# Kernel tuning notes

Measured on AMD Instinct MI355X. Metric: run time of the kernel, lower is better.

Reference implementation:

```python
import jax, jax.numpy as jnp
import numpy as np

B, T, D, H, L, W = 32, 512, 256, 8, 2, 10
NQ = 10000
HD = D // H


def setup_inputs():
    key = jax.random.key(0)
    ks = jax.random.split(key, 16)
    def n(k, shape, s=0.02):
        return jax.random.normal(k, shape, jnp.float32) * s
    return {
        "q": jax.random.randint(ks[0], (B, T), 0, NQ),
        "s": jax.random.randint(ks[1], (B, T), 0, 2),
        "q_embed": n(ks[2], (NQ + 1, D)),
        "s_embed": n(ks[3], (2, D)),
        "pos_embed": n(ks[4], (512, D)),
        "fusion_w": n(ks[5], (2 * D, D)),
        "fusion_b": jnp.zeros((D,), jnp.float32),
        "in_proj_w": n(ks[6], (L, D, 3 * D)),
        "in_proj_b": jnp.zeros((L, 3 * D), jnp.float32),
        "out_proj_w": n(ks[7], (L, D, D)),
        "out_proj_b": jnp.zeros((L, D), jnp.float32),
        "ln1_g": jnp.ones((L, D), jnp.float32),
        "ln1_b": jnp.zeros((L, D), jnp.float32),
        "ln2_g": jnp.ones((L, D), jnp.float32),
        "ln2_b": jnp.zeros((L, D), jnp.float32),
        "ff1_w": n(ks[8], (L, D, 4 * D)),
        "ff1_b": jnp.zeros((L, 4 * D), jnp.float32),
        "ff2_w": n(ks[9], (L, 4 * D, D)),
        "ff2_b": jnp.zeros((L, D), jnp.float32),
        "sw1": n(ks[10], (6, 32), 0.1),
        "sb1": jnp.zeros((32,), jnp.float32),
        "sw2": n(ks[11], (32, D // 4), 0.1),
        "sb2": jnp.zeros((D // 4,), jnp.float32),
        "cw1": n(ks[12], (D + D // 4, D)),
        "cb1": jnp.zeros((D,), jnp.float32),
        "cw2": n(ks[13], (D, 1)),
        "cb2": jnp.zeros((1,), jnp.float32),
    }


def _ln(x, g, b):
    mu = jnp.mean(x, -1, keepdims=True)
    var = jnp.mean(jnp.square(x - mu), -1, keepdims=True)
    return (x - mu) * jax.lax.rsqrt(var + 1e-5) * g + b


def _sliding_sum(x, w):
    # sum over trailing window of size w ending at each t, via prefix sums
    c = jnp.concatenate([jnp.zeros((x.shape[0], 1), x.dtype), jnp.cumsum(x, axis=1)], axis=1)
    t = jnp.arange(x.shape[1])
    return c[:, t + 1] - c[:, jnp.maximum(t + 1 - w, 0)]


def _stats(s, mask):
    # vectorized version of _extract_statistics (prefix-sum sliding windows)
    mf = mask.astype(jnp.float32)
    sf = s.astype(jnp.float32) * mf
    valid = _sliding_sum(mf, W)
    correct_rate = _sliding_sum(sf, W) / (valid + 1e-6)
    rc = _sliding_sum(mf, 5)
    recent_correct = _sliding_sum(sf, 5) / (rc + 1e-6)
    trans = ((s[:, 1:] != s[:, :-1]) & mask[:, 1:] & mask[:, :-1]).astype(jnp.float32)
    diff = jnp.concatenate([jnp.zeros((s.shape[0], 1), jnp.float32), trans], axis=1)
    change_rate = _sliding_sum(diff, W - 1) / (valid + 1e-6)
    # max consecutive equal run within each trailing window of size W
    sp = jnp.pad(s, ((0, 0), (W - 1, 0)))
    mp = jnp.pad(mask, ((0, 0), (W - 1, 0)))
    win_s = [sp[:, j:j + T] for j in range(W)]
    win_m = [mp[:, j:j + T] for j in range(W)]
    run = win_m[0].astype(jnp.float32)
    mx = run
    for j in range(1, W):  # fixed small window, not a data-dim loop
        eq = (win_s[j] == win_s[j - 1]) & win_m[j - 1]
        run = win_m[j].astype(jnp.float32) * (jnp.where(eq, run, 0.0) + 1.0)
        mx = jnp.maximum(mx, run)
    rel = jnp.broadcast_to(jnp.arange(T, dtype=jnp.float32) / max(T, 100), s.shape)
    cov = valid / W
    return jnp.stack([correct_rate, recent_correct, change_rate, mx / W, rel, cov], axis=-1)


def reference(q, s, q_embed, s_embed, pos_embed, fusion_w, fusion_b, in_proj_w, in_proj_b,
              out_proj_w, out_proj_b, ln1_g, ln1_b, ln2_g, ln2_b, ff1_w, ff1_b, ff2_w, ff2_b,
              sw1, sb1, sw2, sb2, cw1, cb1, cw2, cb2):
    mask = s >= 0
    qm = jnp.where(mask, q, 0)
    sm = jnp.where(mask, s, 0)
    h = jnp.concatenate([q_embed[qm], s_embed[sm]], axis=-1)  # [B,T,2D]
    h = jax.nn.relu(h @ fusion_w + fusion_b) + pos_embed[:T][None]
    causal = jnp.tril(jnp.ones((T, T), bool))
    allowed = causal[None, None] & mask[:, None, None, :]
    scale = 1.0 / (HD ** 0.5)
    for l in range(L):
        qkv = h @ in_proj_w[l] + in_proj_b[l]
        qh, kh, vh = jnp.split(qkv, 3, axis=-1)
        qh = qh.reshape(B, T, H, HD).transpose(0, 2, 1, 3)
        kh = kh.reshape(B, T, H, HD).transpose(0, 2, 1, 3)
        vh = vh.reshape(B, T, H, HD).transpose(0, 2, 1, 3)
        scores = jnp.einsum('bhqd,bhkd->bhqk', qh, kh) * scale
        scores = jnp.where(allowed, scores, -1e9)
        attn = jax.nn.softmax(scores, axis=-1)
        o = jnp.einsum('bhqk,bhkd->bhqd', attn, vh).transpose(0, 2, 1, 3).reshape(B, T, D)
        h = _ln(h + (o @ out_proj_w[l] + out_proj_b[l]), ln1_g[l], ln1_b[l])
        ff = jax.nn.gelu(h @ ff1_w[l] + ff1_b[l], approximate=False) @ ff2_w[l] + ff2_b[l]
        h = _ln(h + ff, ln2_g[l], ln2_b[l])
    sfeat = _stats(sm, mask)  # [B,T,6]
    semb = jax.nn.relu(sfeat @ sw1 + sb1) @ sw2 + sb2  # [B,T,D//4]
    comb = jnp.concatenate([h, semb], axis=-1)
    logits = (jax.nn.relu(comb @ cw1 + cb1) @ cw2 + cb2)[..., 0]
    return jnp.where(mask, logits, -1e9)
```

## Files before the change

kernel.cpp:

```cpp
#include <hip/hip_runtime.h>
#include <hip/hip_bf16.h>
#include <cmath>


using short8 = __attribute__((ext_vector_type(8))) short;
using short4v = __attribute__((ext_vector_type(4))) short;
using f32x4  = __attribute__((ext_vector_type(4))) float;

__device__ inline float gelu_f(float x) {
    return 0.5f * x * (1.0f + erff(x * 0.70710678118654752f));
}

__device__ inline short f2bf(float x) {
    union { float f; unsigned u; } v; v.f = x;
    return (short)((v.u + 0x7fffu + ((v.u >> 16) & 1u)) >> 16);
}

__device__ inline float bf2f(short v) {
    union { unsigned u; float f; } x; x.u = ((unsigned)(unsigned short)v) << 16;
    return x.f;
}

__device__ inline unsigned packbf(float lo, float hi) {
    union { float f; unsigned u; } a, b; a.f = lo; b.f = hi;
    unsigned ra = (a.u + 0x7fffu + ((a.u >> 16) & 1u)) >> 16;
    unsigned rb = (b.u + 0x7fffu + ((b.u >> 16) & 1u)) >> 16;
    return (rb << 16) | (ra & 0xffffu);
}

#define GLOAD16(gp, lp) __builtin_amdgcn_global_load_lds( \
    (const __attribute__((address_space(1))) void*)(gp), \
    (__attribute__((address_space(3))) void*)(lp), 16, 0, 0)

__global__ __launch_bounds__(256) void prep_kernel(
    const float* __restrict__ fusion_w, const float* __restrict__ in_proj_w,
    const float* __restrict__ out_proj_w, const float* __restrict__ ff1_w,
    const float* __restrict__ ff2_w, const float* __restrict__ cw1,
    short* __restrict__ wts,
    const int* __restrict__ q, const int* __restrict__ s,
    const float* __restrict__ qe, const float* __restrict__ se,
    short* __restrict__ A)
{
    __shared__ float tile[32][33];
    if (blockIdx.x < 1744) {
        const int b0[10]      = {0,128,320,512,576,640,896,1152,1408,1664};
        const int Ks[10]      = {512,256,256,256,256,256,256,1024,1024,320};
        const int Ns[10]      = {256,768,768,256,256,1024,1024,256,256,256};
        const int sidx[10]    = {0,1,1,2,2,3,3,4,4,5};
        const size_t soff[10] = {0,0,196608,0,65536,0,262144,0,262144,0};
        const size_t doff[10] = {0,131072,327680,524288,589824,655360,917504,1179648,1441792,1703936};
        const float* srcs[6] = {fusion_w, in_proj_w, out_proj_w, ff1_w, ff2_w, cw1};
        int bid = blockIdx.x;
        int mi = 0;
        while (mi < 9 && bid >= b0[mi + 1]) ++mi;
        int bl = bid - b0[mi];
        int K = Ks[mi], N = Ns[mi];
        int tx = bl % (N >> 5), ty = bl / (N >> 5);
        const float* src = srcs[sidx[mi]] + soff[mi];
        short* dst = wts + doff[mi];
        int c = threadIdx.x & 31, r = threadIdx.x >> 5;
#pragma unroll
        for (int i = 0; i < 4; ++i)
            tile[r + i * 8][c] = src[(size_t)(ty * 32 + r + i * 8) * N + tx * 32 + c];
        __syncthreads();
#pragma unroll
        for (int i = 0; i < 4; ++i)
            dst[(size_t)(tx * 32 + r + i * 8) * K + ty * 32 + c] = f2bf(tile[c][r + i * 8]);
    } else {
        int e8 = (blockIdx.x - 1744) * 256 + threadIdx.x;
        int row = e8 >> 6;
        int k8 = (e8 & 63) << 3;
        int sv = s[row];
        bool mk = sv >= 0;
        const float* src = (k8 < 256) ? qe + (size_t)(mk ? q[row] : 0) * 256 + k8
                                      : se + (size_t)(mk ? sv : 0) * 256 + (k8 - 256);
        float4 v0 = *(const float4*)src;
        float4 v1 = *(const float4*)(src + 4);
        short8 o;
        o[0] = f2bf(v0.x); o[1] = f2bf(v0.y); o[2] = f2bf(v0.z); o[3] = f2bf(v0.w);
        o[4] = f2bf(v1.x); o[5] = f2bf(v1.y); o[6] = f2bf(v1.z); o[7] = f2bf(v1.w);
        *(short8*)(A + (size_t)row * 512 + k8) = o;
    }
}

template<int EPI, int BN, int K>
__global__ __launch_bounds__(512) void gemm_bstat(
    const short* __restrict__ A, const short* __restrict__ Wt,
    const float* __restrict__ bias, short* __restrict__ out0,
    short* __restrict__ ok, short* __restrict__ ov,
    const float* __restrict__ pos)
{
    constexpr int SPR = K / 8;
    constexpr int NSTEP = K / 32;
    constexpr int NJ = BN / 16;
    __shared__ short Bs[BN * K];
    const int tid = threadIdx.x, lane = tid & 63, wv = tid >> 6;
    const int lg = lane >> 4, lr = lane & 15;
    const int n0 = blockIdx.y * BN;
    const int row0 = blockIdx.x * 128 + wv * 16;

#pragma unroll
    for (int i = 0; i < (BN * K) / 4096; ++i) {
        int slot = i * 512 + tid;
        int n = slot / SPR, posn = slot % SPR;
        int g = posn ^ (n & 7);
        GLOAD16(Wt + (size_t)(n0 + n) * K + g * 8, &Bs[slot * 8]);
    }
    const short* arow = A + (size_t)(row0 + lr) * K;
    short8 af[NSTEP];
#pragma unroll
    for (int kk = 0; kk < NSTEP; ++kk)
        af[kk] = *(const short8*)(arow + kk * 32 + lg * 8);
    __syncthreads();

    f32x4 acc[NJ] = {};
#pragma unroll
    for (int kk = 0; kk < NSTEP; ++kk) {
#pragma unroll
        for (int j = 0; j < NJ; ++j) {
            int n = j * 16 + lr;
            short8 b = *(const short8*)&Bs[n * K + (((kk * 4 + lg) ^ (n & 7)) << 3)];
            acc[j] = __builtin_amdgcn_mfma_f32_16x16x32_bf16(af[kk], b, acc[j], 0, 0, 0);
        }
    }

    if constexpr (EPI == 0) {
#pragma unroll
        for (int j = 0; j < NJ; ++j)
#pragma unroll
        for (int r = 0; r < 4; ++r) {
            int row = row0 + lg * 4 + r;
            int col = n0 + j * 16 + lr;
            float x = acc[j][r] + bias[col];
            x = fmaxf(x, 0.f) + pos[(size_t)(row & 511) * 256 + col];
            out0[(size_t)row * 256 + col] = f2bf(x);
        }
    } else if constexpr (EPI == 1) {
#pragma unroll
        for (int j = 0; j < NJ; ++j)
#pragma unroll
        for (int r = 0; r < 4; ++r) {
            int row = row0 + lg * 4 + r;
            int gcol = n0 + j * 16 + lr;
            int t = row & 511, bg = row >> 9;
            int sec = gcol >> 8, cc = gcol & 255;
            int h = cc >> 5, d = cc & 31, bh = bg * 8 + h;
            short v = f2bf(acc[j][r] + bias[gcol]);
            if (sec == 0)      out0[((size_t)bh * 512 + t) * 32 + d] = v;
            else if (sec == 1) ok[((size_t)bh * 512 + t) * 32 + d] = v;
            else {
                int kl = t & 31;
                ov[(size_t)bh * 16384 + (size_t)(t >> 5) * 1024 +
                   (size_t)((kl >> 2) & 3) * 256 + d * 8 + (((kl & 3) << 1) | ((kl >> 4) & 1))] = v;
            }
        }
    } else {
#pragma unroll
        for (int j = 0; j < NJ; ++j)
#pragma unroll
        for (int r = 0; r < 4; ++r) {
            int row = row0 + lg * 4 + r;
            int gcol = n0 + j * 16 + lr;
            float x = acc[j][r] + bias[gcol];
            out0[(size_t)row * 1024 + gcol] = f2bf(gelu_f(x));
        }
    }
}

template<int EPI>
__global__ __launch_bounds__(512) void gemm_red(
    const short* __restrict__ A, const short* __restrict__ A2,
    const short* __restrict__ Wt, const float* __restrict__ bias,
    short* __restrict__ hb,
    const float* __restrict__ gamma, const float* __restrict__ beta,
    const float* __restrict__ cw2, const float* __restrict__ cb2,
    const int* __restrict__ smask, float* __restrict__ outlog, int K)
{
    const int tid = threadIdx.x, lane = tid & 63, wv = tid >> 6;
    const int lg = lane >> 4, lr = lane & 15;
    const int wr = wv >> 2, wc = wv & 3;
    const int m0 = blockIdx.x * 64;

    __shared__ short As[2][2048];
    __shared__ short Bs[2][8192];
    __shared__ float redS[64][4];
    __shared__ float redQ[64][4];

    f32x4 acc[2][4] = {};
    const int nsteps = K >> 5;

    auto stage = [&](int buf, int step) {
        int k0 = step << 5;
        if (tid < 256) {
            int k = k0 + wv * 8;
            const short* srcA;
            if constexpr (EPI == 4)
                srcA = (k < 256) ? A + (size_t)(m0 + lane) * 256 + k
                                 : A2 + (size_t)(m0 + lane) * 64 + (k - 256);
            else
                srcA = A + (size_t)(m0 + lane) * K + k;
            GLOAD16(srcA, &As[buf][(wv * 64) * 8]);
        }
        {
            GLOAD16(Wt + (size_t)(tid & 255) * K + k0 + (tid >> 8) * 8,
                    &Bs[buf][(wv * 64) * 8]);
        }
        {
            int slot = tid + 512;
            GLOAD16(Wt + (size_t)(slot & 255) * K + k0 + (slot >> 8) * 8,
                    &Bs[buf][((wv + 8) * 64) * 8]);
        }
    };

    stage(0, 0);
    __syncthreads();
    for (int step = 0; step < nsteps; ++step) {
        int cur = step & 1;
        if (step + 1 < nsteps) stage(cur ^ 1, step + 1);
        short8 a[2], b[4];
#pragma unroll
        for (int i = 0; i < 2; ++i)
            a[i] = *(const short8*)&As[cur][(lg * 64 + wr * 32 + i * 16 + lr) * 8];
#pragma unroll
        for (int j = 0; j < 4; ++j)
            b[j] = *(const short8*)&Bs[cur][(lg * 256 + wc * 64 + j * 16 + lr) * 8];
#pragma unroll
        for (int i = 0; i < 2; ++i)
#pragma unroll
            for (int j = 0; j < 4; ++j)
                acc[i][j] = __builtin_amdgcn_mfma_f32_16x16x32_bf16(a[i], b[j], acc[i][j], 0, 0, 0);
        __syncthreads();
    }

    if constexpr (EPI == 3) {
        float ps[2][4], pq[2][4];
#pragma unroll
        for (int i = 0; i < 2; ++i)
#pragma unroll
        for (int r = 0; r < 4; ++r) { ps[i][r] = 0.f; pq[i][r] = 0.f; }
#pragma unroll
        for (int i = 0; i < 2; ++i)
#pragma unroll
        for (int j = 0; j < 4; ++j)
#pragma unroll
        for (int r = 0; r < 4; ++r) {
            int row = m0 + wr * 32 + i * 16 + lg * 4 + r;
            int col = wc * 64 + j * 16 + lr;
            float x = acc[i][j][r] + bias[col] + bf2f(hb[(size_t)row * 256 + col]);
            acc[i][j][r] = x;
            ps[i][r] += x; pq[i][r] += x * x;
        }
#pragma unroll
        for (int off = 1; off < 16; off <<= 1)
#pragma unroll
            for (int i = 0; i < 2; ++i)
#pragma unroll
            for (int r = 0; r < 4; ++r) {
                ps[i][r] += __shfl_xor(ps[i][r], off);
                pq[i][r] += __shfl_xor(pq[i][r], off);
            }
        if (lr == 0) {
#pragma unroll
            for (int i = 0; i < 2; ++i)
#pragma unroll
            for (int r = 0; r < 4; ++r) {
                int rl = wr * 32 + i * 16 + lg * 4 + r;
                redS[rl][wc] = ps[i][r]; redQ[rl][wc] = pq[i][r];
            }
        }
        __syncthreads();
#pragma unroll
        for (int i = 0; i < 2; ++i)
#pragma unroll
        for (int r = 0; r < 4; ++r) {
            int rl = wr * 32 + i * 16 + lg * 4 + r;
            int row = m0 + rl;
            float sm = redS[rl][0] + redS[rl][1] + redS[rl][2] + redS[rl][3];
            float sq = redQ[rl][0] + redQ[rl][1] + redQ[rl][2] + redQ[rl][3];
            float mu = sm * (1.f / 256.f);
            float var = sq * (1.f / 256.f) - mu * mu;
            float rstd = rsqrtf(var + 1e-5f);
#pragma unroll
            for (int j = 0; j < 4; ++j) {
                int col = wc * 64 + j * 16 + lr;
                float yv = (acc[i][j][r] - mu) * rstd * gamma[col] + beta[col];
                hb[(size_t)row * 256 + col] = f2bf(yv);
            }
        }
    } else {
        float pa[2][4];
#pragma unroll
        for (int i = 0; i < 2; ++i)
#pragma unroll
        for (int r = 0; r < 4; ++r) pa[i][r] = 0.f;
#pragma unroll
        for (int i = 0; i < 2; ++i)
#pragma unroll
        for (int j = 0; j < 4; ++j)
#pragma unroll
        for (int r = 0; r < 4; ++r) {
            int col = wc * 64 + j * 16 + lr;
            float x = fmaxf(acc[i][j][r] + bias[col], 0.f);
            pa[i][r] += x * cw2[col];
        }
#pragma unroll
        for (int off = 1; off < 16; off <<= 1)
#pragma unroll
            for (int i = 0; i < 2; ++i)
#pragma unroll
            for (int r = 0; r < 4; ++r) pa[i][r] += __shfl_xor(pa[i][r], off);
        if (lr == 0) {
#pragma unroll
            for (int i = 0; i < 2; ++i)
#pragma unroll
            for (int r = 0; r < 4; ++r)
                redS[wr * 32 + i * 16 + lg * 4 + r][wc] = pa[i][r];
        }
        __syncthreads();
        if (tid < 64) {
            int row = m0 + tid;
            float v = redS[tid][0] + redS[tid][1] + redS[tid][2] + redS[tid][3] + cb2[0];
            outlog[row] = (smask[row] >= 0) ? v : -1e9f;
        }
    }
}

__global__ __launch_bounds__(256) void attn_mfma(
    const short* __restrict__ Qg, const short* __restrict__ Kg,
    const short* __restrict__ VTg, short* __restrict__ O)
{
    __shared__ unsigned Wp[4][16][20];
    const int bh = blockIdx.x >> 2, part = blockIdx.x & 3;
    const int b = bh >> 3, h = bh & 7;
    const int wv = threadIdx.x >> 6, lane = threadIdx.x & 63;
    const int lg = lane >> 4, lr = lane & 15;
    const int slot = part * 4 + wv;
    const short* Qbh = Qg + (size_t)bh * 16384;
    const short* Kbh = Kg + (size_t)bh * 16384;
    const short* Vbh = VTg + (size_t)bh * 16384;
    const float scale = 0.17677669529663687f;

    for (int half = 0; half < 2; ++half) {
        const int tile = half ? (31 - slot) : slot;
        const int q0 = tile << 4;
        short8 qa = *(const short8*)(Qbh + (size_t)(q0 + lr) * 32 + lg * 8);
        f32x4 o0 = {}, o1 = {};
        float l_[4] = {0.f, 0.f, 0.f, 0.f};
        const int nfull = q0 >> 5;

        for (int c = 0; c <= nfull; ++c) {
            int kc = c << 5;
            short8 kf0 = *(const short8*)(Kbh + (size_t)(kc + lr) * 32 + lg * 8);
            short8 kf1 = *(const short8*)(Kbh + (size_t)(kc + 16 + lr) * 32 + lg * 8);
            f32x4 s0 = {}, s1 = {};
            s0 = __builtin_amdgcn_mfma_f32_16x16x32_bf16(qa, kf0, s0, 0, 0, 0);
            s1 = __builtin_amdgcn_mfma_f32_16x16x32_bf16(qa, kf1, s1, 0, 0, 0);
            float p0[4], p1[4];
            if (c < nfull) {
#pragma unroll
                for (int r = 0; r < 4; ++r) {
                    p0[r] = __expf(s0[r] * scale);
                    p1[r] = __expf(s1[r] * scale);
                }
            } else {
#pragma unroll
                for (int r = 0; r < 4; ++r) {
                    int qq = q0 + lg * 4 + r;
                    p0[r] = (kc + lr)      > qq ? 0.f : __expf(s0[r] * scale);
                    p1[r] = (kc + 16 + lr) > qq ? 0.f : __expf(s1[r] * scale);
                }
            }
#pragma unroll
            for (int r = 0; r < 4; ++r) {
                l_[r] += p0[r] + p1[r];
                Wp[wv][lg * 4 + r][lr] = packbf(p0[r], p1[r]);
            }
            short8 pa = *(const short8*)&Wp[wv][lr][lg * 4];
            short8 vf0 = *(const short8*)(Vbh + (size_t)c * 1024 + lg * 256 + lr * 8);
            short8 vf1 = *(const short8*)(Vbh + (size_t)c * 1024 + lg * 256 + (lr + 16) * 8);
            o0 = __builtin_amdgcn_mfma_f32_16x16x32_bf16(pa, vf0, o0, 0, 0, 0);
            o1 = __builtin_amdgcn_mfma_f32_16x16x32_bf16(pa, vf1, o1, 0, 0, 0);
        }
#pragma unroll
        for (int off = 1; off < 16; off <<= 1)
#pragma unroll
            for (int r = 0; r < 4; ++r) l_[r] += __shfl_xor(l_[r], off);
#pragma unroll
        for (int r = 0; r < 4; ++r) {
            float inv = 1.f / l_[r];
            size_t ro = ((size_t)b * 512 + q0 + lg * 4 + r) * 256 + h * 32;
            O[ro + lr] = f2bf(o0[r] * inv);
            O[ro + 16 + lr] = f2bf(o1[r] * inv);
        }
    }
}

__global__ __launch_bounds__(512) void stats_kernel(
    const int* __restrict__ s, short* __restrict__ semb,
    const float* __restrict__ sw1, const float* __restrict__ sb1,
    const float* __restrict__ sw2, const float* __restrict__ sb2)
{
    __shared__ float sv_sh[512];
    __shared__ float m_sh[512];
    __shared__ float sw2_sh[2048];
    const int b = blockIdx.x;
    const int t = threadIdx.x;
    {
        int sval = s[b * 512 + t];
        bool mk = sval >= 0;
        sv_sh[t] = mk ? (float)sval : 0.f;
        m_sh[t] = mk ? 1.f : 0.f;
    }
    for (int i = t; i < 2048; i += 512) sw2_sh[i] = sw2[i];
    __syncthreads();

    float mf10 = 0, sf10 = 0, mf5 = 0, sf5 = 0, d9 = 0;
#pragma unroll
    for (int k = 0; k < 10; ++k) {
        int idx = t - k;
        if (idx >= 0) {
            float mv = m_sh[idx], sv = sv_sh[idx];
            mf10 += mv; sf10 += sv;
            if (k < 5) { mf5 += mv; sf5 += sv; }
            if (k < 9 && idx >= 1) {
                if (sv != sv_sh[idx - 1] && mv > 0.5f && m_sh[idx - 1] > 0.5f) d9 += 1.f;
            }
        }
    }
    float run, mx;
    {
        int x0 = t - 9;
        run = (x0 >= 0) ? m_sh[x0] : 0.f;
        mx = run;
#pragma unroll
        for (int j = 1; j < 10; ++j) {
            int xc = t + j - 9, xp = xc - 1;
            float sc = (xc >= 0) ? sv_sh[xc] : 0.f;
            float sp = (xp >= 0) ? sv_sh[xp] : 0.f;
            float mc = (xc >= 0) ? m_sh[xc] : 0.f;
            float mp = (xp >= 0) ? m_sh[xp] : 0.f;
            bool eq = (sc == sp) && (mp > 0.5f);
            run = (mc > 0.5f) ? ((eq ? run : 0.f) + 1.f) : 0.f;
            mx = fmaxf(mx, run);
        }
    }
    float f[6];
    f[0] = sf10 / (mf10 + 1e-6f);
    f[1] = sf5 / (mf5 + 1e-6f);
    f[2] = d9 / (mf10 + 1e-6f);
    f[3] = mx * 0.1f;
    f[4] = (float)t * (1.f / 512.f);
    f[5] = mf10 * 0.1f;

    float hid[32];
#pragma unroll
    for (int j2 = 0; j2 < 32; ++j2) {
        float a = sb1[j2];
#pragma unroll
        for (int i = 0; i < 6; ++i) a = fmaf(f[i], sw1[i * 32 + j2], a);
        hid[j2] = fmaxf(a, 0.f);
    }
    short* orow = semb + ((size_t)b * 512 + t) * 64;
    for (int c = 0; c < 64; c += 4) {
        float v0 = sb2[c], v1 = sb2[c + 1], v2 = sb2[c + 2], v3 = sb2[c + 3];
#pragma unroll
        for (int j2 = 0; j2 < 32; ++j2) {
            float hh = hid[j2];
            v0 = fmaf(hh, sw2_sh[j2 * 64 + c], v0);
            v1 = fmaf(hh, sw2_sh[j2 * 64 + c + 1], v1);
            v2 = fmaf(hh, sw2_sh[j2 * 64 + c + 2], v2);
            v3 = fmaf(hh, sw2_sh[j2 * 64 + c + 3], v3);
        }
        short4v o; o[0] = f2bf(v0); o[1] = f2bf(v1); o[2] = f2bf(v2); o[3] = f2bf(v3);
        *(short4v*)(orow + c) = o;
    }
}

extern "C" void kernel_launch(void* const* d_in, const int* in_sizes, int n_in,
                              void* d_out, int out_size, void* d_ws, size_t ws_size,
                              hipStream_t stream) {
    const int*   q         = (const int*)d_in[0];
    const int*   s         = (const int*)d_in[1];
    const float* q_embed   = (const float*)d_in[2];
    const float* s_embed   = (const float*)d_in[3];
    const float* pos_embed = (const float*)d_in[4];
    const float* fusion_w  = (const float*)d_in[5];
    const float* fusion_b  = (const float*)d_in[6];
    const float* in_proj_w = (const float*)d_in[7];
    const float* in_proj_b = (const float*)d_in[8];
    const float* out_proj_w= (const float*)d_in[9];
    const float* out_proj_b= (const float*)d_in[10];
    const float* ln1_g     = (const float*)d_in[11];
    const float* ln1_b     = (const float*)d_in[12];
    const float* ln2_g     = (const float*)d_in[13];
    const float* ln2_b     = (const float*)d_in[14];
    const float* ff1_w     = (const float*)d_in[15];
    const float* ff1_b     = (const float*)d_in[16];
    const float* ff2_w     = (const float*)d_in[17];
    const float* ff2_b     = (const float*)d_in[18];
    const float* sw1       = (const float*)d_in[19];
    const float* sb1       = (const float*)d_in[20];
    const float* sw2       = (const float*)d_in[21];
    const float* sb2       = (const float*)d_in[22];
    const float* cw1       = (const float*)d_in[23];
    const float* cb1       = (const float*)d_in[24];
    const float* cw2       = (const float*)d_in[25];
    const float* cb2       = (const float*)d_in[26];
    float* out = (float*)d_out;

    char* base = (char*)d_ws;
    short* hb   = (short*)(base);
    short* bufA = (short*)(base + 8388608);
    short* att  = (short*)(base + 41943040);
    short* Qg   = (short*)(base + 50331648);
    short* Kg   = (short*)(base + 58720256);
    short* VTg  = (short*)(base + 67108864);
    short* semb = (short*)(base + 75497472);
    short* wts  = (short*)(base + 77594624);

    const size_t W_FUSION = 0, W_INPROJ0 = 131072, W_INPROJ1 = 327680;
    const size_t W_OUTPROJ0 = 524288, W_OUTPROJ1 = 589824;
    const size_t W_FF1_0 = 655360, W_FF1_1 = 917504;
    const size_t W_FF2_0 = 1179648, W_FF2_1 = 1441792;
    const size_t W_CW1 = 1703936;

    prep_kernel<<<5840, 256, 0, stream>>>(fusion_w, in_proj_w, out_proj_w,
                                          ff1_w, ff2_w, cw1, wts,
                                          q, s, q_embed, s_embed, bufA);
    gemm_bstat<0, 64, 512><<<dim3(128, 4), 512, 0, stream>>>(bufA,
        wts + W_FUSION, fusion_b, hb, nullptr, nullptr, pos_embed);
    for (int l = 0; l < 2; ++l) {
        gemm_bstat<1, 128, 256><<<dim3(128, 6), 512, 0, stream>>>(hb,
            wts + (l ? W_INPROJ1 : W_INPROJ0), in_proj_b + l * 768,
            Qg, Kg, VTg, nullptr);
        attn_mfma<<<1024, 256, 0, stream>>>(Qg, Kg, VTg, att);
        gemm_red<3><<<256, 512, 0, stream>>>(att, nullptr,
            wts + (l ? W_OUTPROJ1 : W_OUTPROJ0), out_proj_b + l * 256,
            hb, ln1_g + l * 256, ln1_b + l * 256,
            nullptr, nullptr, nullptr, nullptr, 256);
        gemm_bstat<2, 128, 256><<<dim3(128, 8), 512, 0, stream>>>(hb,
            wts + (l ? W_FF1_1 : W_FF1_0), ff1_b + l * 1024,
            bufA, nullptr, nullptr, nullptr);
        gemm_red<3><<<256, 512, 0, stream>>>(bufA, nullptr,
            wts + (l ? W_FF2_1 : W_FF2_0), ff2_b + l * 256,
            hb, ln2_g + l * 256, ln2_b + l * 256,
            nullptr, nullptr, nullptr, nullptr, 1024);
    }
    stats_kernel<<<32, 512, 0, stream>>>(s, semb, sw1, sb1, sw2, sb2);
    gemm_red<4><<<256, 512, 0, stream>>>(hb, semb,
        wts + W_CW1, cb1, nullptr, nullptr, nullptr,
        cw2, cb2, s, out, 320);
}
```

Baseline: 281.4 us.

## Unify GEMMs into one column-split kernel, split LayerNorm out, fold stats into prep

Replaces the row-block gemm_red kernels, which fused residual add and LayerNorm across the full 256-wide rows, with a single generic MFMA GEMM using 64-column tiles and K chunked through LDS. LayerNorm now runs as a separate kernel over an fp32 residual buffer, and the classifier head writes per-column-tile partial dot products that a small final kernel reduces and masks. The stats MLP moves into extra blocks of the prep kernel, and the QKV and FF1 GEMMs use narrower tiles with more blocks. The aim is more parallelism and one fewer launch, at the cost of extra fp32 round-trips through global memory and two extra launches per layer.

Result: slower. 289.8 us (+3.0%).

```diff
diff --git a/kernel.cpp b/kernel.cpp
--- a/kernel.cpp
+++ b/kernel.cpp
@@ -32,16 +32,23 @@
     (const __attribute__((address_space(1))) void*)(gp), \
     (__attribute__((address_space(3))) void*)(lp), 16, 0, 0)
 
-__global__ __launch_bounds__(256) void prep_kernel(
+__global__ __launch_bounds__(256) void prep(
     const float* __restrict__ fusion_w, const float* __restrict__ in_proj_w,
     const float* __restrict__ out_proj_w, const float* __restrict__ ff1_w,
     const float* __restrict__ ff2_w, const float* __restrict__ cw1,
     short* __restrict__ wts,
     const int* __restrict__ q, const int* __restrict__ s,
     const float* __restrict__ qe, const float* __restrict__ se,
-    short* __restrict__ A)
+    short* __restrict__ A,
+    short* __restrict__ semb,
+    const float* __restrict__ sw1, const float* __restrict__ sb1,
+    const float* __restrict__ sw2, const float* __restrict__ sb2)
 {
     __shared__ float tile[32][33];
+    __shared__ float sv_sh[512];
+    __shared__ float m_sh[512];
+    __shared__ float sw2_sh[2048];
+
     if (blockIdx.x < 1744) {
         const int b0[10]      = {0,128,320,512,576,640,896,1152,1408,1664};
         const int Ks[10]      = {512,256,256,256,256,256,256,1024,1024,320};
@@ -66,7 +73,7 @@
 #pragma unroll
         for (int i = 0; i < 4; ++i)
             dst[(size_t)(tx * 32 + r + i * 8) * K + ty * 32 + c] = f2bf(tile[c][r + i * 8]);
-    } else {
+    } else if (blockIdx.x < 5840) {
         int e8 = (blockIdx.x - 1744) * 256 + threadIdx.x;
         int row = e8 >> 6;
         int k8 = (e8 & 63) << 3;
@@ -80,64 +87,153 @@
         o[0] = f2bf(v0.x); o[1] = f2bf(v0.y); o[2] = f2bf(v0.z); o[3] = f2bf(v0.w);
         o[4] = f2bf(v1.x); o[5] = f2bf(v1.y); o[6] = f2bf(v1.z); o[7] = f2bf(v1.w);
         *(short8*)(A + (size_t)row * 512 + k8) = o;
-    }
-}
-
-template<int EPI, int BN, int K>
-__global__ __launch_bounds__(512) void gemm_bstat(
-    const short* __restrict__ A, const short* __restrict__ Wt,
-    const float* __restrict__ bias, short* __restrict__ out0,
-    short* __restrict__ ok, short* __restrict__ ov,
-    const float* __restrict__ pos)
+    } else {
+        const int b = blockIdx.x - 5840;
+        const int tt = threadIdx.x;
+        for (int t = tt; t < 512; t += 256) {
+            int sval = s[b * 512 + t];
+            bool mk = sval >= 0;
+            sv_sh[t] = mk ? (float)sval : 0.f;
+            m_sh[t] = mk ? 1.f : 0.f;
+        }
+        for (int i = tt; i < 2048; i += 256) sw2_sh[i] = sw2[i];
+        __syncthreads();
+        for (int half = 0; half < 2; ++half) {
+            const int t = tt + half * 256;
+            float mf10 = 0, sf10 = 0, mf5 = 0, sf5 = 0, d9 = 0;
+#pragma unroll
+            for (int k = 0; k < 10; ++k) {
+                int idx = t - k;
+                if (idx >= 0) {
+                    float mv = m_sh[idx], sv = sv_sh[idx];
+                    mf10 += mv; sf10 += sv;
+                    if (k < 5) { mf5 += mv; sf5 += sv; }
+                    if (k < 9 && idx >= 1) {
+                        if (sv != sv_sh[idx - 1] && mv > 0.5f && m_sh[idx - 1] > 0.5f) d9 += 1.f;
+                    }
+                }
+            }
+            float run, mx;
+            {
+                int x0 = t - 9;
+                run = (x0 >= 0) ? m_sh[x0] : 0.f;
+                mx = run;
+#pragma unroll
+                for (int j = 1; j < 10; ++j) {
+                    int xc = t + j - 9, xp = xc - 1;
+                    float sc = (xc >= 0) ? sv_sh[xc] : 0.f;
+                    float sp = (xp >= 0) ? sv_sh[xp] : 0.f;
+                    float mc = (xc >= 0) ? m_sh[xc] : 0.f;
+                    float mp = (xp >= 0) ? m_sh[xp] : 0.f;
+                    bool eq = (sc == sp) && (mp > 0.5f);
+                    run = (mc > 0.5f) ? ((eq ? run : 0.f) + 1.f) : 0.f;
+                    mx = fmaxf(mx, run);
+                }
+            }
+            float f[6];
+            f[0] = sf10 / (mf10 + 1e-6f);
+            f[1] = sf5 / (mf5 + 1e-6f);
+            f[2] = d9 / (mf10 + 1e-6f);
+            f[3] = mx * 0.1f;
+            f[4] = (float)t * (1.f / 512.f);
+            f[5] = mf10 * 0.1f;
+
+            float hid[32];
+#pragma unroll
+            for (int j2 = 0; j2 < 32; ++j2) {
+                float a = sb1[j2];
+#pragma unroll
+                for (int i = 0; i < 6; ++i) a = fmaf(f[i], sw1[i * 32 + j2], a);
+                hid[j2] = fmaxf(a, 0.f);
+            }
+            short* orow = semb + ((size_t)b * 512 + t) * 64;
+            for (int c = 0; c < 64; c += 4) {
+                float v0 = sb2[c], v1 = sb2[c + 1], v2 = sb2[c + 2], v3 = sb2[c + 3];
+#pragma unroll
+                for (int j2 = 0; j2 < 32; ++j2) {
+                    float hh = hid[j2];
+                    v0 = fmaf(hh, sw2_sh[j2 * 64 + c], v0);
+                    v1 = fmaf(hh, sw2_sh[j2 * 64 + c + 1], v1);
+                    v2 = fmaf(hh, sw2_sh[j2 * 64 + c + 2], v2);
+                    v3 = fmaf(hh, sw2_sh[j2 * 64 + c + 3], v3);
+                }
+                short4v o; o[0] = f2bf(v0); o[1] = f2bf(v1); o[2] = f2bf(v2); o[3] = f2bf(v3);
+                *(short4v*)(orow + c) = o;
+            }
+        }
+    }
+}
+
+template<int EPI, int KTOT>
+__global__ __launch_bounds__(512) void kbs(
+    const short* __restrict__ A, const short* __restrict__ A2,
+    const short* __restrict__ Wt, const float* __restrict__ bias,
+    short* __restrict__ o0, short* __restrict__ o1, short* __restrict__ o2,
+    float* __restrict__ xb, short* __restrict__ hb,
+    const float* __restrict__ pos, const float* __restrict__ cw2v,
+    float* __restrict__ pbuf)
 {
-    constexpr int SPR = K / 8;
-    constexpr int NSTEP = K / 32;
-    constexpr int NJ = BN / 16;
-    __shared__ short Bs[BN * K];
+    constexpr int BN = 64;
+    constexpr int NCH = (KTOT + 255) / 256;
+    constexpr int KA = (EPI == 4) ? 256 : KTOT;
+    __shared__ short Bs[BN * 256];
     const int tid = threadIdx.x, lane = tid & 63, wv = tid >> 6;
     const int lg = lane >> 4, lr = lane & 15;
     const int n0 = blockIdx.y * BN;
     const int row0 = blockIdx.x * 128 + wv * 16;
 
-#pragma unroll
-    for (int i = 0; i < (BN * K) / 4096; ++i) {
-        int slot = i * 512 + tid;
-        int n = slot / SPR, posn = slot % SPR;
-        int g = posn ^ (n & 7);
-        GLOAD16(Wt + (size_t)(n0 + n) * K + g * 8, &Bs[slot * 8]);
-    }
-    const short* arow = A + (size_t)(row0 + lr) * K;
-    short8 af[NSTEP];
-#pragma unroll
-    for (int kk = 0; kk < NSTEP; ++kk)
-        af[kk] = *(const short8*)(arow + kk * 32 + lg * 8);
-    __syncthreads();
-
-    f32x4 acc[NJ] = {};
-#pragma unroll
-    for (int kk = 0; kk < NSTEP; ++kk) {
-#pragma unroll
-        for (int j = 0; j < NJ; ++j) {
-            int n = j * 16 + lr;
-            short8 b = *(const short8*)&Bs[n * K + (((kk * 4 + lg) ^ (n & 7)) << 3)];
-            acc[j] = __builtin_amdgcn_mfma_f32_16x16x32_bf16(af[kk], b, acc[j], 0, 0, 0);
+    f32x4 acc[4] = {};
+    short8 af[8];
+
+#pragma unroll
+    for (int c = 0; c < NCH; ++c) {
+        const int ck = (KTOT - c * 256 >= 256) ? 256 : (KTOT - c * 256);
+        const int spr = ck >> 3;
+        if (c) __syncthreads();
+        for (int i = 0; i < (BN * ck) / 8; i += 512) {
+            int slot = i + tid;
+            int n = slot / spr, posn = slot % spr;
+            int g = posn ^ (n & 7);
+            GLOAD16(Wt + (size_t)(n0 + n) * KTOT + c * 256 + g * 8, &Bs[slot * 8]);
+        }
+        const int nkk = ck >> 5;
+        if (EPI == 4 && c == 1) {
+            const short* ar2 = A2 + (size_t)(row0 + lr) * 64 + lg * 8;
+            af[0] = *(const short8*)(ar2);
+            af[1] = *(const short8*)(ar2 + 32);
+        } else {
+            const short* ar = A + (size_t)(row0 + lr) * KA + c * 256 + lg * 8;
+#pragma unroll
+            for (int kk = 0; kk < 8; ++kk)
+                if (kk < nkk) af[kk] = *(const short8*)(ar + kk * 32);
+        }
+        __syncthreads();
+#pragma unroll
+        for (int kk = 0; kk < 8; ++kk) {
+            if (kk >= nkk) break;
+#pragma unroll
+            for (int j = 0; j < 4; ++j) {
+                int n = j * 16 + lr;
+                short8 b = *(const short8*)&Bs[n * ck + (((kk * 4 + lg) ^ (n & 7)) << 3)];
+                acc[j] = __builtin_amdgcn_mfma_f32_16x16x32_bf16(af[kk], b, acc[j], 0, 0, 0);
+            }
         }
     }
 
     if constexpr (EPI == 0) {
 #pragma unroll
-        for (int j = 0; j < NJ; ++j)
+        for (int j = 0; j < 4; ++j)
 #pragma unroll
         for (int r = 0; r < 4; ++r) {
             int row = row0 + lg * 4 + r;
             int col = n0 + j * 16 + lr;
             float x = acc[j][r] + bias[col];
             x = fmaxf(x, 0.f) + pos[(size_t)(row & 511) * 256 + col];
-            out0[(size_t)row * 256 + col] = f2bf(x);
+            o0[(size_t)row * 256 + col] = f2bf(x);
         }
     } else if constexpr (EPI == 1) {
 #pragma unroll
-        for (int j = 0; j < NJ; ++j)
+        for (int j = 0; j < 4; ++j)
 #pragma unroll
         for (int r = 0; r < 4; ++r) {
             int row = row0 + lg * 4 + r;
@@ -146,183 +242,89 @@
             int sec = gcol >> 8, cc = gcol & 255;
             int h = cc >> 5, d = cc & 31, bh = bg * 8 + h;
             short v = f2bf(acc[j][r] + bias[gcol]);
-            if (sec == 0)      out0[((size_t)bh * 512 + t) * 32 + d] = v;
-            else if (sec == 1) ok[((size_t)bh * 512 + t) * 32 + d] = v;
+            if (sec == 0)      o0[((size_t)bh * 512 + t) * 32 + d] = v;
+            else if (sec == 1) o1[((size_t)bh * 512 + t) * 32 + d] = v;
             else {
                 int kl = t & 31;
-                ov[(size_t)bh * 16384 + (size_t)(t >> 5) * 1024 +
+                o2[(size_t)bh * 16384 + (size_t)(t >> 5) * 1024 +
                    (size_t)((kl >> 2) & 3) * 256 + d * 8 + (((kl & 3) << 1) | ((kl >> 4) & 1))] = v;
             }
         }
-    } else {
-#pragma unroll
-        for (int j = 0; j < NJ; ++j)
+    } else if constexpr (EPI == 2) {
+#pragma unroll
+        for (int j = 0; j < 4; ++j)
 #pragma unroll
         for (int r = 0; r < 4; ++r) {
             int row = row0 + lg * 4 + r;
             int gcol = n0 + j * 16 + lr;
             float x = acc[j][r] + bias[gcol];
-            out0[(size_t)row * 1024 + gcol] = f2bf(gelu_f(x));
-        }
-    }
-}
-
-template<int EPI>
-__global__ __launch_bounds__(512) void gemm_red(
-    const short* __restrict__ A, const short* __restrict__ A2,
-    const short* __restrict__ Wt, const float* __restrict__ bias,
-    short* __restrict__ hb,
-    const float* __restrict__ gamma, const float* __restrict__ beta,
-    const float* __restrict__ cw2, const float* __restrict__ cb2,
-    const int* __restrict__ smask, float* __restrict__ outlog, int K)
+            o0[(size_t)row * 1024 + gcol] = f2bf(gelu_f(x));
+        }
+    } else if constexpr (EPI == 3) {
+#pragma unroll
+        for (int j = 0; j < 4; ++j)
+#pragma unroll
+        for (int r = 0; r < 4; ++r) {
+            int row = row0 + lg * 4 + r;
+            int col = n0 + j * 16 + lr;
+            xb[(size_t)row * 256 + col] =
+                acc[j][r] + bias[col] + bf2f(hb[(size_t)row * 256 + col]);
+        }
+    } else {
+#pragma unroll
+        for (int r = 0; r < 4; ++r) {
+            float p = 0.f;
+#pragma unroll
+            for (int j = 0; j < 4; ++j) {
+                int col = n0 + j * 16 + lr;
+                float v = fmaxf(acc[j][r] + bias[col], 0.f);
+                p += v * cw2v[col];
+            }
+#pragma unroll
+            for (int off = 1; off < 16; off <<= 1) p += __shfl_xor(p, off);
+            if (lr == 0) {
+                int row = row0 + lg * 4 + r;
+                pbuf[(size_t)blockIdx.y * 16384 + row] = p;
+            }
+        }
+    }
+}
+
+__global__ __launch_bounds__(256) void k_ln(
+    const float* __restrict__ xb, short* __restrict__ hb,
+    const float* __restrict__ gamma, const float* __restrict__ beta)
 {
-    const int tid = threadIdx.x, lane = tid & 63, wv = tid >> 6;
-    const int lg = lane >> 4, lr = lane & 15;
-    const int wr = wv >> 2, wc = wv & 3;
-    const int m0 = blockIdx.x * 64;
-
-    __shared__ short As[2][2048];
-    __shared__ short Bs[2][8192];
-    __shared__ float redS[64][4];
-    __shared__ float redQ[64][4];
-
-    f32x4 acc[2][4] = {};
-    const int nsteps = K >> 5;
-
-    auto stage = [&](int buf, int step) {
-        int k0 = step << 5;
-        if (tid < 256) {
-            int k = k0 + wv * 8;
-            const short* srcA;
-            if constexpr (EPI == 4)
-                srcA = (k < 256) ? A + (size_t)(m0 + lane) * 256 + k
-                                 : A2 + (size_t)(m0 + lane) * 64 + (k - 256);
-            else
-                srcA = A + (size_t)(m0 + lane) * K + k;
-            GLOAD16(srcA, &As[buf][(wv * 64) * 8]);
-        }
-        {
-            GLOAD16(Wt + (size_t)(tid & 255) * K + k0 + (tid >> 8) * 8,
-                    &Bs[buf][(wv * 64) * 8]);
-        }
-        {
-            int slot = tid + 512;
-            GLOAD16(Wt + (size_t)(slot & 255) * K + k0 + (slot >> 8) * 8,
-                    &Bs[buf][((wv + 8) * 64) * 8]);
-        }
-    };
-
-    stage(0, 0);
-    __syncthreads();
-    for (int step = 0; step < nsteps; ++step) {
-        int cur = step & 1;
-        if (step + 1 < nsteps) stage(cur ^ 1, step + 1);
-        short8 a[2], b[4];
-#pragma unroll
-        for (int i = 0; i < 2; ++i)
-            a[i] = *(const short8*)&As[cur][(lg * 64 + wr * 32 + i * 16 + lr) * 8];
-#pragma unroll
-        for (int j = 0; j < 4; ++j)
-            b[j] = *(const short8*)&Bs[cur][(lg * 256 + wc * 64 + j * 16 + lr) * 8];
-#pragma unroll
-        for (int i = 0; i < 2; ++i)
-#pragma unroll
-            for (int j = 0; j < 4; ++j)
-                acc[i][j] = __builtin_amdgcn_mfma_f32_16x16x32_bf16(a[i], b[j], acc[i][j], 0, 0, 0);
-        __syncthreads();
-    }
-
-    if constexpr (EPI == 3) {
-        float ps[2][4], pq[2][4];
-#pragma unroll
-        for (int i = 0; i < 2; ++i)
-#pragma unroll
-        for (int r = 0; r < 4; ++r) { ps[i][r] = 0.f; pq[i][r] = 0.f; }
-#pragma unroll
-        for (int i = 0; i < 2; ++i)
-#pragma unroll
-        for (int j = 0; j < 4; ++j)
-#pragma unroll
-        for (int r = 0; r < 4; ++r) {
-            int row = m0 + wr * 32 + i * 16 + lg * 4 + r;
-            int col = wc * 64 + j * 16 + lr;
-            float x = acc[i][j][r] + bias[col] + bf2f(hb[(size_t)row * 256 + col]);
-            acc[i][j][r] = x;
-            ps[i][r] += x; pq[i][r] += x * x;
-        }
-#pragma unroll
-        for (int off = 1; off < 16; off <<= 1)
-#pragma unroll
-            for (int i = 0; i < 2; ++i)
-#pragma unroll
-            for (int r = 0; r < 4; ++r) {
-                ps[i][r] += __shfl_xor(ps[i][r], off);
-                pq[i][r] += __shfl_xor(pq[i][r], off);
-            }
-        if (lr == 0) {
-#pragma unroll
-            for (int i = 0; i < 2; ++i)
-#pragma unroll
-            for (int r = 0; r < 4; ++r) {
-                int rl = wr * 32 + i * 16 + lg * 4 + r;
-                redS[rl][wc] = ps[i][r]; redQ[rl][wc] = pq[i][r];
-            }
-        }
-        __syncthreads();
-#pragma unroll
-        for (int i = 0; i < 2; ++i)
-#pragma unroll
-        for (int r = 0; r < 4; ++r) {
-            int rl = wr * 32 + i * 16 + lg * 4 + r;
-            int row = m0 + rl;
-            float sm = redS[rl][0] + redS[rl][1] + redS[rl][2] + redS[rl][3];
-            float sq = redQ[rl][0] + redQ[rl][1] + redQ[rl][2] + redQ[rl][3];
-            float mu = sm * (1.f / 256.f);
-            float var = sq * (1.f / 256.f) - mu * mu;
-            float rstd = rsqrtf(var + 1e-5f);
-#pragma unroll
-            for (int j = 0; j < 4; ++j) {
-                int col = wc * 64 + j * 16 + lr;
-                float yv = (acc[i][j][r] - mu) * rstd * gamma[col] + beta[col];
-                hb[(size_t)row * 256 + col] = f2bf(yv);
-            }
-        }
-    } else {
-        float pa[2][4];
-#pragma unroll
-        for (int i = 0; i < 2; ++i)
-#pragma unroll
-        for (int r = 0; r < 4; ++r) pa[i][r] = 0.f;
-#pragma unroll
-        for (int i = 0; i < 2; ++i)
-#pragma unroll
-        for (int j = 0; j < 4; ++j)
-#pragma unroll
-        for (int r = 0; r < 4; ++r) {
-            int col = wc * 64 + j * 16 + lr;
-            float x = fmaxf(acc[i][j][r] + bias[col], 0.f);
-            pa[i][r] += x * cw2[col];
-        }
-#pragma unroll
-        for (int off = 1; off < 16; off <<= 1)
-#pragma unroll
-            for (int i = 0; i < 2; ++i)
-#pragma unroll
-            for (int r = 0; r < 4; ++r) pa[i][r] += __shfl_xor(pa[i][r], off);
-        if (lr == 0) {
-#pragma unroll
-            for (int i = 0; i < 2; ++i)
-#pragma unroll
-            for (int r = 0; r < 4; ++r)
-                redS[wr * 32 + i * 16 + lg * 4 + r][wc] = pa[i][r];
-        }
-        __syncthreads();
-        if (tid < 64) {
-            int row = m0 + tid;
-            float v = redS[tid][0] + redS[tid][1] + redS[tid][2] + redS[tid][3] + cb2[0];
-            outlog[row] = (smask[row] >= 0) ? v : -1e9f;
-        }
-    }
+    int row = blockIdx.x * 4 + (threadIdx.x >> 6);
+    int lane = threadIdx.x & 63;
+    int c = lane * 4;
+    float4 xv = *reinterpret_cast<const float4*>(xb + (size_t)row * 256 + c);
+    float sm = xv.x + xv.y + xv.z + xv.w;
+    float sq = xv.x * xv.x + xv.y * xv.y + xv.z * xv.z + xv.w * xv.w;
+#pragma unroll
+    for (int off = 32; off > 0; off >>= 1) {
+        sm += __shfl_xor(sm, off);
+        sq += __shfl_xor(sq, off);
+    }
+    float mu = sm * (1.f / 256.f);
+    float var = sq * (1.f / 256.f) - mu * mu;
+    float rstd = rsqrtf(var + 1e-5f);
+    float4 gv = *reinterpret_cast<const float4*>(gamma + c);
+    float4 bv = *reinterpret_cast<const float4*>(beta + c);
+    short4v o;
+    o[0] = f2bf((xv.x - mu) * rstd * gv.x + bv.x);
+    o[1] = f2bf((xv.y - mu) * rstd * gv.y + bv.y);
+    o[2] = f2bf((xv.z - mu) * rstd * gv.z + bv.z);
+    o[3] = f2bf((xv.w - mu) * rstd * gv.w + bv.w);
+    *(short4v*)(hb + (size_t)row * 256 + c) = o;
+}
+
+__global__ __launch_bounds__(256) void k_fin(
+    const float* __restrict__ pbuf, const int* __restrict__ s,
+    const float* __restrict__ cb2, float* __restrict__ out)
+{
+    int i = blockIdx.x * 256 + threadIdx.x;
+    float v = pbuf[i] + pbuf[i + 16384] + pbuf[i + 32768] + pbuf[i + 49152] + cb2[0];
+    out[i] = (s[i] >= 0) ? v : -1e9f;
 }
 
 __global__ __launch_bounds__(256) void attn_mfma(
@@ -392,87 +394,6 @@
             O[ro + lr] = f2bf(o0[r] * inv);
             O[ro + 16 + lr] = f2bf(o1[r] * inv);
         }
-    }
-}
-
-__global__ __launch_bounds__(512) void stats_kernel(
-    const int* __restrict__ s, short* __restrict__ semb,
-    const float* __restrict__ sw1, const float* __restrict__ sb1,
-    const float* __restrict__ sw2, const float* __restrict__ sb2)
-{
-    __shared__ float sv_sh[512];
-    __shared__ float m_sh[512];
-    __shared__ float sw2_sh[2048];
-    const int b = blockIdx.x;
-    const int t = threadIdx.x;
-    {
-        int sval = s[b * 512 + t];
-        bool mk = sval >= 0;
-        sv_sh[t] = mk ? (float)sval : 0.f;
-        m_sh[t] = mk ? 1.f : 0.f;
-    }
-    for (int i = t; i < 2048; i += 512) sw2_sh[i] = sw2[i];
-    __syncthreads();
-
-    float mf10 = 0, sf10 = 0, mf5 = 0, sf5 = 0, d9 = 0;
-#pragma unroll
-    for (int k = 0; k < 10; ++k) {
-        int idx = t - k;
-        if (idx >= 0) {
-            float mv = m_sh[idx], sv = sv_sh[idx];
-            mf10 += mv; sf10 += sv;
-            if (k < 5) { mf5 += mv; sf5 += sv; }
-            if (k < 9 && idx >= 1) {
-                if (sv != sv_sh[idx - 1] && mv > 0.5f && m_sh[idx - 1] > 0.5f) d9 += 1.f;
-            }
-        }
-    }
-    float run, mx;
-    {
-        int x0 = t - 9;
-        run = (x0 >= 0) ? m_sh[x0] : 0.f;
-        mx = run;
-#pragma unroll
-        for (int j = 1; j < 10; ++j) {
-            int xc = t + j - 9, xp = xc - 1;
-            float sc = (xc >= 0) ? sv_sh[xc] : 0.f;
-            float sp = (xp >= 0) ? sv_sh[xp] : 0.f;
-            float mc = (xc >= 0) ? m_sh[xc] : 0.f;
-            float mp = (xp >= 0) ? m_sh[xp] : 0.f;
-            bool eq = (sc == sp) && (mp > 0.5f);
-            run = (mc > 0.5f) ? ((eq ? run : 0.f) + 1.f) : 0.f;
-            mx = fmaxf(mx, run);
-        }
-    }
-    float f[6];
-    f[0] = sf10 / (mf10 + 1e-6f);
-    f[1] = sf5 / (mf5 + 1e-6f);
-    f[2] = d9 / (mf10 + 1e-6f);
-    f[3] = mx * 0.1f;
-    f[4] = (float)t * (1.f / 512.f);
-    f[5] = mf10 * 0.1f;
-
-    float hid[32];
-#pragma unroll
-    for (int j2 = 0; j2 < 32; ++j2) {
-        float a = sb1[j2];
-#pragma unroll
-        for (int i = 0; i < 6; ++i) a = fmaf(f[i], sw1[i * 32 + j2], a);
-        hid[j2] = fmaxf(a, 0.f);
-    }
-    short* orow = semb + ((size_t)b * 512 + t) * 64;
-    for (int c = 0; c < 64; c += 4) {
-        float v0 = sb2[c], v1 = sb2[c + 1], v2 = sb2[c + 2], v3 = sb2[c + 3];
-#pragma unroll
-        for (int j2 = 0; j2 < 32; ++j2) {
-            float hh = hid[j2];
-            v0 = fmaf(hh, sw2_sh[j2 * 64 + c], v0);
-            v1 = fmaf(hh, sw2_sh[j2 * 64 + c + 1], v1);
-            v2 = fmaf(hh, sw2_sh[j2 * 64 + c + 2], v2);
-            v3 = fmaf(hh, sw2_sh[j2 * 64 + c + 3], v3);
-        }
-        short4v o; o[0] = f2bf(v0); o[1] = f2bf(v1); o[2] = f2bf(v2); o[3] = f2bf(v3);
-        *(short4v*)(orow + c) = o;
     }
 }
 
@@ -517,6 +438,8 @@
     short* VTg  = (short*)(base + 67108864);
     short* semb = (short*)(base + 75497472);
     short* wts  = (short*)(base + 77594624);
+    float* xb   = (float*)(base + 81166336);
+    float* pbuf = (float*)(base + 97943552);
 
     const size_t W_FUSION = 0, W_INPROJ0 = 131072, W_INPROJ1 = 327680;
     const size_t W_OUTPROJ0 = 524288, W_OUTPROJ1 = 589824;
@@ -524,30 +447,32 @@
     const size_t W_FF2_0 = 1179648, W_FF2_1 = 1441792;
     const size_t W_CW1 = 1703936;
 
-    prep_kernel<<<5840, 256, 0, stream>>>(fusion_w, in_proj_w, out_proj_w,
-                                          ff1_w, ff2_w, cw1, wts,
-                                          q, s, q_embed, s_embed, bufA);
-    gemm_bstat<0, 64, 512><<<dim3(128, 4), 512, 0, stream>>>(bufA,
-        wts + W_FUSION, fusion_b, hb, nullptr, nullptr, pos_embed);
+    prep<<<5872, 256, 0, stream>>>(fusion_w, in_proj_w, out_proj_w,
+                                   ff1_w, ff2_w, cw1, wts,
+                                   q, s, q_embed, s_embed, bufA,
+                                   semb, sw1, sb1, sw2, sb2);
+    kbs<0, 512><<<dim3(128, 4), 512, 0, stream>>>(bufA, nullptr,
+        wts + W_FUSION, fusion_b, hb, nullptr, nullptr, nullptr, nullptr,
+        pos_embed, nullptr, nullptr);
     for (int l = 0; l < 2; ++l) {
-        gemm_bstat<1, 128, 256><<<dim3(128, 6), 512, 0, stream>>>(hb,
+        kbs<1, 256><<<dim3(128, 12), 512, 0, stream>>>(hb, nullptr,
             wts + (l ? W_INPROJ1 : W_INPROJ0), in_proj_b + l * 768,
-            Qg, Kg, VTg, nullptr);
+            Qg, Kg, VTg, nullptr, nullptr, nullptr, nullptr, nullptr);
         attn_mfma<<<1024, 256, 0, stream>>>(Qg, Kg, VTg, att);
-        gemm_red<3><<<256, 512, 0, stream>>>(att, nullptr,
+        kbs<3, 256><<<dim3(128, 4), 512, 0, stream>>>(att, nullptr,
             wts + (l ? W_OUTPROJ1 : W_OUTPROJ0), out_proj_b + l * 256,
-            hb, ln1_g + l * 256, ln1_b + l * 256,
-            nullptr, nullptr, nullptr, nullptr, 256);
-        gemm_bstat<2, 128, 256><<<dim3(128, 8), 512, 0, stream>>>(hb,
+            nullptr, nullptr, nullptr, xb, hb, nullptr, nullptr, nullptr);
+        k_ln<<<4096, 256, 0, stream>>>(xb, hb, ln1_g + l * 256, ln1_b + l * 256);
+        kbs<2, 256><<<dim3(128, 16), 512, 0, stream>>>(hb, nullptr,
             wts + (l ? W_FF1_1 : W_FF1_0), ff1_b + l * 1024,
-            bufA, nullptr, nullptr, nullptr);
-        gemm_red<3><<<256, 512, 0, stream>>>(bufA, nullptr,
+            bufA, nullptr, nullptr, nullptr, nullptr, nullptr, nullptr, nullptr);
+        kbs<3, 1024><<<dim3(128, 4), 512, 0, stream>>>(bufA, nullptr,
             wts + (l ? W_FF2_1 : W_FF2_0), ff2_b + l * 256,
-            hb, ln2_g + l * 256, ln2_b + l * 256,
-            nullptr, nullptr, nullptr, nullptr, 1024);
-    }
-    stats_kernel<<<32, 512, 0, stream>>>(s, semb, sw1, sb1, sw2, sb2);
-    gemm_red<4><<<256, 512, 0, stream>>>(hb, semb,
-        wts + W_CW1, cb1, nullptr, nullptr, nullptr,
-        cw2, cb2, s, out, 320);
-}
+            nullptr, nullptr, nullptr, xb, hb, nullptr, nullptr, nullptr);
+        k_ln<<<4096, 256, 0, stream>>>(xb, hb, ln2_g + l * 256, ln2_b + l * 256);
+    }
+    kbs<4, 320><<<dim3(128, 4), 512, 0, stream>>>(hb, semb,
+        wts + W_CW1, cb1, nullptr, nullptr, nullptr, nullptr, nullptr,
+        nullptr, cw2, pbuf);
+    k_fin<<<64, 256, 0, stream>>>(pbuf, s, cb2, out);
+}
```
